# Kernel optimization log

Hardware: AMD Instinct MI355X
Metric: run time of the kernel (lower is better)

Reference implementation:

```python
import jax, jax.numpy as jnp
import numpy as np

N_NODES = 50000
N_EDGES = 800000
F_IN = 128
HEADS = 4
C_OUT = 32
NEG_SLOPE = 0.2
BN_EPS = 1e-5


def _add_self_loops(edge_index, edge_attr, n):
    # PyG fill_value='mean': self-loop attr = mean of incoming edge attrs per node (0 if none)
    src, dst = edge_index[0], edge_index[1]
    deg = jax.ops.segment_sum(jnp.ones_like(edge_attr[:, 0]), dst, num_segments=n)
    loop_attr = jax.ops.segment_sum(edge_attr, dst, num_segments=n) / jnp.maximum(deg, 1.0)[:, None]
    loop = jnp.arange(n)
    src2 = jnp.concatenate([src, loop])
    dst2 = jnp.concatenate([dst, loop])
    attr2 = jnp.concatenate([edge_attr, loop_attr], axis=0)
    return src2, dst2, attr2


def _segment_softmax(logits, seg, n):
    m = jax.ops.segment_max(logits, seg, num_segments=n)
    m = jnp.where(jnp.isfinite(m), m, 0.0)
    ex = jnp.exp(logits - m[seg])
    s = jax.ops.segment_sum(ex, seg, num_segments=n)
    return ex / s[seg]


def _gatv2(x, src, dst, eattr, Wl, bl, Wr, br, We, att, bias, n):
    # x: [n, F]; returns [n, HEADS*C_OUT]
    xl = (x @ Wl + bl).reshape(n, HEADS, C_OUT)
    xr = (x @ Wr + br).reshape(n, HEADS, C_OUT)
    ea = (eattr @ We).reshape(-1, HEADS, C_OUT)
    xlj = xl[src]                                   # [E, H, C] gather
    msg = jax.nn.leaky_relu(xlj + xr[dst] + ea, NEG_SLOPE)
    logits = jnp.einsum('ehc,hc->eh', msg, att)     # [E, H]
    alpha = _segment_softmax(logits, dst, n)
    out = jax.ops.segment_sum(xlj * alpha[..., None], dst, num_segments=n)
    return out.reshape(n, HEADS * C_OUT) + bias


def _batchnorm(x, gamma, beta):
    mu = x.mean(axis=0)
    var = x.var(axis=0)
    return gamma * (x - mu) * jax.lax.rsqrt(var + BN_EPS) + beta


def setup_inputs() -> dict:
    key = jax.random.key(0)
    ks = jax.random.split(key, 20)
    HC = HEADS * C_OUT
    s = 0.05
    inp = {
        'emb': jax.random.normal(ks[0], (N_NODES, F_IN), dtype=jnp.float32),
        'edge_index': jax.random.randint(ks[1], (2, N_EDGES), 0, N_NODES, dtype=jnp.int64),
        'edge_weight': jax.random.uniform(ks[2], (N_EDGES, 1), dtype=jnp.float32),
        'Wl1': jax.random.normal(ks[3], (F_IN, HC)) * s,
        'bl1': jnp.zeros((HC,), jnp.float32),
        'Wr1': jax.random.normal(ks[4], (F_IN, HC)) * s,
        'br1': jnp.zeros((HC,), jnp.float32),
        'We1': jax.random.normal(ks[5], (1, HC)) * s,
        'att1': jax.random.normal(ks[6], (HEADS, C_OUT)) * s,
        'bias1': jnp.zeros((HC,), jnp.float32),
        'gamma1': jnp.ones((HC,), jnp.float32),
        'beta1': jnp.zeros((HC,), jnp.float32),
        'Wl2': jax.random.normal(ks[7], (HC, HC)) * s,
        'bl2': jnp.zeros((HC,), jnp.float32),
        'Wr2': jax.random.normal(ks[8], (HC, HC)) * s,
        'br2': jnp.zeros((HC,), jnp.float32),
        'We2': jax.random.normal(ks[9], (1, HC)) * s,
        'att2': jax.random.normal(ks[10], (HEADS, C_OUT)) * s,
        'bias2': jnp.zeros((HC,), jnp.float32),
    }
    return inp


def reference(emb, edge_index, edge_weight, Wl1, bl1, Wr1, br1, We1, att1, bias1,
              gamma1, beta1, Wl2, bl2, Wr2, br2, We2, att2, bias2):
    n = emb.shape[0]
    src, dst, eattr = _add_self_loops(edge_index, edge_weight, n)
    h1 = _gatv2(emb, src, dst, eattr, Wl1, bl1, Wr1, br1, We1, att1, bias1, n)
    h1 = jax.nn.elu(_batchnorm(h1, gamma1, beta1))
    h2 = _gatv2(h1, src, dst, eattr, Wl2, bl2, Wr2, br2, We2, att2, bias2, n)
    # fusion: mean over [input_emb, h1, h2] along stacked axis
    return (emb + h1 + h2) / 3.0
```

## Files before the change

kernel.cpp:

```cpp
#include <hip/hip_runtime.h>
#include <hip/hip_bf16.h>
#include <math.h>

#define N_NODES 50000
#define N_EDGES 800000
#define HC 128
#define SLOT 64

#define BM 128
#define NBX ((N_NODES + BM - 1) / BM)
#define NCHK 64
#define EPB (N_EDGES / NCHK)
#define NRNG 4
#define RNG_N (N_NODES / NRNG)
#define RNG_W (RNG_N / 2)
#define NW (N_NODES / 2)
#define NSCAT (NCHK * NRNG)

typedef short bh8 __attribute__((ext_vector_type(8)));
typedef float f4 __attribute__((ext_vector_type(4)));
typedef float f2 __attribute__((ext_vector_type(2)));

__device__ __forceinline__ unsigned int pk2(float a, float b) {
  return (unsigned int)__bfloat16_as_ushort(__float2bfloat16(a)) |
         ((unsigned int)__bfloat16_as_ushort(__float2bfloat16(b)) << 16);
}
__device__ __forceinline__ float blo(unsigned int u) { return __uint_as_float(u << 16); }
__device__ __forceinline__ float bhi(unsigned int u) { return __uint_as_float(u & 0xffff0000u); }
__device__ __forceinline__ f2 vmax2(f2 a, f2 b) {
#if __has_builtin(__builtin_elementwise_max)
  return __builtin_elementwise_max(a, b);
#else
  f2 r; r.x = fmaxf(a.x, b.x); r.y = fmaxf(a.y, b.y); return r;
#endif
}

__global__ __launch_bounds__(256) void k_histprep(
    const float* __restrict__ Wl1, const float* __restrict__ Wr1,
    const float* __restrict__ Wl2, const float* __restrict__ Wr2,
    unsigned short* __restrict__ WtAll,
    float* __restrict__ chsum, float* __restrict__ chsq,
    const int* __restrict__ ei, unsigned int* __restrict__ counts32) {
  __shared__ unsigned int hist[RNG_W];
  int tid = threadIdx.x, bid = blockIdx.x;
  int gid = bid * 256 + tid;
  {
    int m = gid >> 14;
    int idx = gid & 16383;
    const float* src = (m == 0) ? Wl1 : (m == 1) ? Wr1 : (m == 2) ? Wl2 : Wr2;
    int k = idx >> 7, n = idx & 127;
    WtAll[((size_t)m * HC + n) * HC + k] =
        __bfloat16_as_ushort(__float2bfloat16(src[k * HC + n]));
    if (gid < HC) { chsum[gid] = 0.f; chsq[gid] = 0.f; }
  }
  int c = bid >> 2, r = bid & 3;
  int rb = r * RNG_N;
  for (int w = tid; w < RNG_W; w += 256) hist[w] = 0u;
  __syncthreads();
  const int* dstp = ei + N_EDGES + c * EPB;
  for (int g = tid; g < EPB / 4; g += 256) {
    int4 d4 = *(const int4*)(dstp + g * 4);
    int dl;
    dl = d4.x - rb; if ((unsigned)dl < RNG_N) atomicAdd(&hist[dl >> 1], (dl & 1) ? 0x10000u : 1u);
    dl = d4.y - rb; if ((unsigned)dl < RNG_N) atomicAdd(&hist[dl >> 1], (dl & 1) ? 0x10000u : 1u);
    dl = d4.z - rb; if ((unsigned)dl < RNG_N) atomicAdd(&hist[dl >> 1], (dl & 1) ? 0x10000u : 1u);
    dl = d4.w - rb; if ((unsigned)dl < RNG_N) atomicAdd(&hist[dl >> 1], (dl & 1) ? 0x10000u : 1u);
  }
  __syncthreads();
  unsigned int* dst = counts32 + (size_t)c * NW + r * RNG_W;
  for (int w = tid; w < RNG_W; w += 256) dst[w] = hist[w];
}

__global__ __launch_bounds__(256) void k_scan(const unsigned int* __restrict__ counts32,
                                              unsigned int* __restrict__ bases32,
                                              int* __restrict__ cursor) {
  int w = blockIdx.x * 256 + threadIdx.x;
  if (w >= NW) return;
  unsigned int a0 = 0, a1 = 0;
#pragma unroll 4
  for (int b = 0; b < NCHK; ++b) {
    unsigned int v = counts32[(size_t)b * NW + w];
    bases32[(size_t)b * NW + w] = a0 | (a1 << 16);
    a0 += v & 0xffffu;
    a1 += v >> 16;
  }
  cursor[2 * w] = (int)a0;
  cursor[2 * w + 1] = (int)a1;
}

__global__ __launch_bounds__(256) void k_scat_g1(
    const int* __restrict__ ei, const float* __restrict__ ew,
    const unsigned int* __restrict__ bases32, unsigned int* __restrict__ slots,
    const float* __restrict__ X, const unsigned short* __restrict__ Wt,
    const float* __restrict__ b0, const float* __restrict__ b1,
    unsigned short* __restrict__ Y0b, float* __restrict__ Y1) {
  __shared__ __align__(16) unsigned int lsbuf[16384];
  int tid = threadIdx.x, bid = blockIdx.x;
  if (bid < NSCAT) {
    int c = bid >> 2, r = bid & 3;
    int rb = r * RNG_N;
    const unsigned int* bp = bases32 + (size_t)c * NW + r * RNG_W;
    for (int w = tid; w < RNG_W; w += 256) lsbuf[w] = bp[w];
    __syncthreads();
    const int* sp = ei + c * EPB;
    const int* dp = ei + N_EDGES + c * EPB;
    const float* wp = ew + c * EPB;
    for (int g = tid; g < EPB / 4; g += 256) {
      int4 s4 = *(const int4*)(sp + g * 4);
      int4 d4 = *(const int4*)(dp + g * 4);
      float4 w4 = *(const float4*)(wp + g * 4);
      int ss[4] = {s4.x, s4.y, s4.z, s4.w};
      int dd[4] = {d4.x, d4.y, d4.z, d4.w};
      float ww[4] = {w4.x, w4.y, w4.z, w4.w};
#pragma unroll
      for (int i = 0; i < 4; ++i) {
        int dl = dd[i] - rb;
        if ((unsigned)dl < RNG_N) {
          unsigned int old = atomicAdd(&lsbuf[dl >> 1], (dl & 1) ? 0x10000u : 1u);
          unsigned int pos = (dl & 1) ? (old >> 16) : (old & 0xffffu);
          unsigned int wq = min((unsigned int)(ww[i] * 65536.f + 0.5f), 65535u);
          if (pos < SLOT)
            slots[(size_t)dd[i] * SLOT + pos] = ((unsigned int)ss[i] << 16) | wq;
        }
      }
    }
    return;
  }
  unsigned short* Xls = (unsigned short*)lsbuf;
  unsigned short* Wls = Xls + 128 * 128;
  int row0 = (bid - NSCAT) * BM;
  {
    int r = tid >> 1;
    int ks = (tid & 1) * 64;
    int gr = row0 + r;
    const float* xp = X + (size_t)gr * HC + ks;
    int sw = r & 15;
#pragma unroll
    for (int i = 0; i < 4; ++i) {
      float f[16];
      if (gr < N_NODES) {
        *(float4*)&f[0] = *(const float4*)(xp + i * 16);
        *(float4*)&f[4] = *(const float4*)(xp + i * 16 + 4);
        *(float4*)&f[8] = *(const float4*)(xp + i * 16 + 8);
        *(float4*)&f[12] = *(const float4*)(xp + i * 16 + 12);
      } else {
#pragma unroll
        for (int j = 0; j < 16; ++j) f[j] = 0.f;
      }
      int kg = (ks >> 3) + i * 2;
      *(uint4*)&Xls[r * 128 + ((kg ^ sw) * 8)] =
          make_uint4(pk2(f[0], f[1]), pk2(f[2], f[3]), pk2(f[4], f[5]), pk2(f[6], f[7]));
      *(uint4*)&Xls[r * 128 + (((kg + 1) ^ sw) * 8)] =
          make_uint4(pk2(f[8], f[9]), pk2(f[10], f[11]), pk2(f[12], f[13]), pk2(f[14], f[15]));
    }
  }
  int lane = tid & 63;
  int wv = tid >> 6;
  int lrow = lane & 15;
  int lq = lane >> 4;
  int rbase = wv * 32;
#pragma unroll
  for (int half = 0; half < 2; ++half) {
    if (half) __syncthreads();
    {
      int n = tid >> 1;
      int ks2 = (tid & 1) * 64;
      const unsigned short* wp = Wt + half * (HC * HC) + n * HC + ks2;
      int swn = n & 15;
#pragma unroll
      for (int g = 0; g < 8; ++g) {
        uint4 v = *(const uint4*)(wp + g * 8);
        int kg = (ks2 >> 3) + g;
        *(uint4*)&Wls[n * 128 + ((kg ^ swn) * 8)] = v;
      }
    }
    __syncthreads();
    f4 acc[2][8];
#pragma unroll
    for (int mt = 0; mt < 2; ++mt)
#pragma unroll
      for (int nt = 0; nt < 8; ++nt) acc[mt][nt] = (f4){0.f, 0.f, 0.f, 0.f};
#pragma unroll
    for (int kk = 0; kk < 4; ++kk) {
      int kg = kk * 4 + lq;
      bh8 a0 = *(const bh8*)&Xls[(rbase + lrow) * 128 + ((kg ^ lrow) * 8)];
      bh8 a1 = *(const bh8*)&Xls[(rbase + 16 + lrow) * 128 + ((kg ^ lrow) * 8)];
#pragma unroll
      for (int nt = 0; nt < 8; ++nt) {
        bh8 b = *(const bh8*)&Wls[(nt * 16 + lrow) * 128 + ((kg ^ lrow) * 8)];
        acc[0][nt] = __builtin_amdgcn_mfma_f32_16x16x32_bf16(a0, b, acc[0][nt], 0, 0, 0);
        acc[1][nt] = __builtin_amdgcn_mfma_f32_16x16x32_bf16(a1, b, acc[1][nt], 0, 0, 0);
      }
    }
    const float* bb = half ? b1 : b0;
    float bv[8];
#pragma unroll
    for (int nt = 0; nt < 8; ++nt) bv[nt] = bb[nt * 16 + lrow];
#pragma unroll
    for (int mt = 0; mt < 2; ++mt) {
#pragma unroll
      for (int rr = 0; rr < 4; ++rr) {
        int gr = row0 + rbase + mt * 16 + lq * 4 + rr;
        if (gr < N_NODES) {
          if (half == 0) {
#pragma unroll
            for (int nt = 0; nt < 8; ++nt)
              Y0b[(size_t)gr * HC + nt * 16 + lrow] =
                  __bfloat16_as_ushort(__float2bfloat16(acc[mt][nt][rr] + bv[nt]));
          } else {
#pragma unroll
            for (int nt = 0; nt < 8; ++nt)
              Y1[(size_t)gr * HC + nt * 16 + lrow] = acc[mt][nt][rr] + bv[nt];
          }
        }
      }
    }
  }
}

__global__ __launch_bounds__(256) void k_gemm2(
    const unsigned short* __restrict__ Xb, const unsigned short* __restrict__ Wt,
    const float* __restrict__ b0, const float* __restrict__ b1,
    unsigned char* __restrict__ Y0f8, float* __restrict__ Y1,
    const float* __restrict__ chsum, const float* __restrict__ chsq,
    const float* __restrict__ gamma, const float* __restrict__ beta) {
  __shared__ __align__(16) unsigned short Xls[128 * 128];
  __shared__ __align__(16) unsigned short Wls[128 * 128];
  __shared__ float ssc[HC], ssh[HC];
  int tid = threadIdx.x;
  if (tid < HC) {
    float mu = chsum[tid] * (1.f / N_NODES);
    float var = chsq[tid] * (1.f / N_NODES) - mu * mu;
    float sc = gamma[tid] * rsqrtf(var + 1e-5f);
    ssc[tid] = sc;
    ssh[tid] = beta[tid] - mu * sc;
  }
  __syncthreads();
  int row0 = blockIdx.x * BM;
  {
    int r = tid >> 1;
    int ks = (tid & 1) * 64;
    int gr = row0 + r;
    const unsigned short* xp = Xb + (size_t)gr * HC + ks;
    int sw = r & 15;
#pragma unroll
    for (int i = 0; i < 4; ++i) {
      float f[16];
      if (gr < N_NODES) {
        uint4 ua = *(const uint4*)(xp + i * 16);
        uint4 ub = *(const uint4*)(xp + i * 16 + 8);
        f[0] = blo(ua.x); f[1] = bhi(ua.x); f[2] = blo(ua.y); f[3] = bhi(ua.y);
        f[4] = blo(ua.z); f[5] = bhi(ua.z); f[6] = blo(ua.w); f[7] = bhi(ua.w);
        f[8] = blo(ub.x); f[9] = bhi(ub.x); f[10] = blo(ub.y); f[11] = bhi(ub.y);
        f[12] = blo(ub.z); f[13] = bhi(ub.z); f[14] = blo(ub.w); f[15] = bhi(ub.w);
      } else {
#pragma unroll
        for (int j = 0; j < 16; ++j) f[j] = 0.f;
      }
#pragma unroll
      for (int j = 0; j < 16; ++j) {
        float y = fmaf(f[j], ssc[ks + i * 16 + j], ssh[ks + i * 16 + j]);
        f[j] = (y > 0.f) ? y : (__expf(y) - 1.f);
      }
      int kg = (ks >> 3) + i * 2;
      *(uint4*)&Xls[r * 128 + ((kg ^ sw) * 8)] =
          make_uint4(pk2(f[0], f[1]), pk2(f[2], f[3]), pk2(f[4], f[5]), pk2(f[6], f[7]));
      *(uint4*)&Xls[r * 128 + (((kg + 1) ^ sw) * 8)] =
          make_uint4(pk2(f[8], f[9]), pk2(f[10], f[11]), pk2(f[12], f[13]), pk2(f[14], f[15]));
    }
  }
  int lane = tid & 63;
  int wv = tid >> 6;
  int lrow = lane & 15;
  int lq = lane >> 4;
  int rbase = wv * 32;
#pragma unroll
  for (int half = 0; half < 2; ++half) {
    if (half) __syncthreads();
    {
      int n = tid >> 1;
      int ks = (tid & 1) * 64;
      const unsigned short* wp = Wt + half * (HC * HC) + n * HC + ks;
      int swn = n & 15;
#pragma unroll
      for (int g = 0; g < 8; ++g) {
        uint4 v = *(const uint4*)(wp + g * 8);
        int kg = (ks >> 3) + g;
        *(uint4*)&Wls[n * 128 + ((kg ^ swn) * 8)] = v;
      }
    }
    __syncthreads();
    f4 acc[2][8];
#pragma unroll
    for (int mt = 0; mt < 2; ++mt)
#pragma unroll
      for (int nt = 0; nt < 8; ++nt) acc[mt][nt] = (f4){0.f, 0.f, 0.f, 0.f};
#pragma unroll
    for (int kk = 0; kk < 4; ++kk) {
      int kg = kk * 4 + lq;
      bh8 a0 = *(const bh8*)&Xls[(rbase + lrow) * 128 + ((kg ^ lrow) * 8)];
      bh8 a1 = *(const bh8*)&Xls[(rbase + 16 + lrow) * 128 + ((kg ^ lrow) * 8)];
#pragma unroll
      for (int nt = 0; nt < 8; ++nt) {
        bh8 b = *(const bh8*)&Wls[(nt * 16 + lrow) * 128 + ((kg ^ lrow) * 8)];
        acc[0][nt] = __builtin_amdgcn_mfma_f32_16x16x32_bf16(a0, b, acc[0][nt], 0, 0, 0);
        acc[1][nt] = __builtin_amdgcn_mfma_f32_16x16x32_bf16(a1, b, acc[1][nt], 0, 0, 0);
      }
    }
    const float* bb = half ? b1 : b0;
    float bv[8];
#pragma unroll
    for (int nt = 0; nt < 8; ++nt) bv[nt] = bb[nt * 16 + lrow];
#pragma unroll
    for (int mt = 0; mt < 2; ++mt) {
#pragma unroll
      for (int rr = 0; rr < 4; ++rr) {
        int gr = row0 + rbase + mt * 16 + lq * 4 + rr;
        if (gr < N_NODES) {
          if (half == 0) {
#pragma unroll
            for (int nt = 0; nt < 8; ++nt) {
              float v = acc[mt][nt][rr] + bv[nt];
              int p = __builtin_amdgcn_cvt_pk_fp8_f32(v, v, 0, false);
              Y0f8[(size_t)gr * HC + nt * 16 + lrow] = (unsigned char)(p & 0xff);
            }
          } else {
#pragma unroll
            for (int nt = 0; nt < 8; ++nt)
              Y1[(size_t)gr * HC + nt * 16 + lrow] = acc[mt][nt][rr] + bv[nt];
          }
        }
      }
    }
  }
}

template <int FINAL, int F8>
__global__ __launch_bounds__(256) void k_gat(
    const void* __restrict__ xlv, const float* __restrict__ xr,
    const int* __restrict__ cursor, const unsigned int* __restrict__ slots,
    const float* __restrict__ We, const float* __restrict__ att,
    const float* __restrict__ bias, void* __restrict__ out,
    const float* __restrict__ emb, const unsigned short* __restrict__ h1p,
    const float* __restrict__ chsum, const float* __restrict__ chsq,
    const float* __restrict__ gamma, const float* __restrict__ beta) {
  int g = threadIdx.x >> 5;
  int lane = threadIdx.x & 31;
  int n = blockIdx.x * 8 + g;
  int fi = n * 32 + lane;
  const uint2* xl2 = (const uint2*)xlv;
  const unsigned int* xf = (const unsigned int*)xlv;
  float4 xr4 = ((const float4*)xr)[fi];
  float4 we4 = ((const float4*)We)[lane];
  float4 at4 = ((const float4*)att)[lane];
  const float LOG2E = 1.4426950408889634f;
  f2 xr01 = {xr4.x, xr4.y}, xr23 = {xr4.z, xr4.w};
  f2 we01 = {we4.x, we4.y}, we23 = {we4.z, we4.w};
  f2 at01 = {at4.x * LOG2E, at4.y * LOG2E}, at23 = {at4.z * LOG2E, at4.w * LOG2E};
  int deg = min(cursor[n], SLOT);
  int base = n * SLOT;
  int deg32 = min(deg, 32);

  unsigned int ev = (lane < deg32) ? slots[base + lane] : 0u;
  float evw = (float)(ev & 0xffffu) * (1.f / 65536.f);
  float wsum = evw;
#pragma unroll
  for (int m = 16; m >= 1; m >>= 1) wsum += __shfl_xor(wsum, m);

  float l = 0.f;
  f2 o01 = {0.f, 0.f}, o23 = {0.f, 0.f};

  auto decode = [&](uint2 gc, f2& a, f2& b) {
    if (F8) {
      a = __builtin_amdgcn_cvt_pk_f32_fp8((int)gc.x, false);
      b = __builtin_amdgcn_cvt_pk_f32_fp8((int)gc.x, true);
    } else {
      a = (f2){blo(gc.x), bhi(gc.x)};
      b = (f2){blo(gc.y), bhi(gc.y)};
    }
  };
  auto edge_body = [&](float w, uint2 gc, bool valid) {
    f2 a, b;
    decode(gc, a, b);
    f2 m01 = (a + xr01) + w * we01;
    f2 m23 = (b + xr23) + w * we23;
    m01 = vmax2(m01, m01 * 0.2f);
    m23 = vmax2(m23, m23 * 0.2f);
    f2 dp = m01 * at01 + m23 * at23;
    float p = dp.x + dp.y;
    p += __shfl_xor(p, 1);
    p += __shfl_xor(p, 2);
    p += __shfl_xor(p, 4);
#if __has_builtin(__builtin_amdgcn_exp2f)
    float e = valid ? __builtin_amdgcn_exp2f(p) : 0.f;
#else
    float e = valid ? __expf(p * 0.6931471805599453f) : 0.f;
#endif
    l += e;
    o01 = o01 + e * a;
    o23 = o23 + e * b;
  };
  auto fetch = [&](int j, uint2& qq, float& ww) {
    int jc = min(j, deg32 - 1);
    unsigned int evj = __shfl(ev, jc, 32);
    ww = (float)(evj & 0xffffu) * (1.f / 65536.f);
    int s = (int)(evj >> 16);
    if (F8) qq.x = xf[s * 32 + lane];
    else qq = xl2[s * 32 + lane];
  };

  if (deg32 > 0) {
    uint2 q0, q1, q2, q3;
    float w0, w1, w2, w3;
    fetch(0, q0, w0);
    fetch(1, q1, w1);
    fetch(2, q2, w2);
    fetch(3, q3, w3);
    for (int b = 0; b < deg32; b += 4) {
      uint2 c0 = q0, c1 = q1, c2 = q2, c3 = q3;
      float x0 = w0, x1 = w1, x2 = w2, x3 = w3;
      fetch(b + 4, q0, w0);
      fetch(b + 5, q1, w1);
      fetch(b + 6, q2, w2);
      fetch(b + 7, q3, w3);
      edge_body(x0, c0, true);
      edge_body(x1, c1, b + 1 < deg32);
      edge_body(x2, c2, b + 2 < deg32);
      edge_body(x3, c3, b + 3 < deg32);
    }
  }
  if (deg > 32) {
    for (int j = base + 32; j < base + deg; ++j) {
      unsigned int evj = slots[j];
      float w = (float)(evj & 0xffffu) * (1.f / 65536.f);
      wsum += w;
      int s = (int)(evj >> 16);
      uint2 gc;
      if (F8) gc.x = xf[s * 32 + lane];
      else gc = xl2[s * 32 + lane];
      edge_body(w, gc, true);
    }
  }
  {
    float wself = (deg > 0) ? wsum / (float)deg : 0.f;
    uint2 gs;
    if (F8) gs.x = xf[n * 32 + lane];
    else gs = xl2[n * 32 + lane];
    edge_body(wself, gs, true);
  }

  float inv = 1.f / l;
  float4 o = make_float4(o01.x, o01.y, o23.x, o23.y);
  float4 b4 = ((const float4*)bias)[lane];
  float4 r;
  r.x = fmaf(o.x, inv, b4.x);
  r.y = fmaf(o.y, inv, b4.y);
  r.z = fmaf(o.z, inv, b4.z);
  r.w = fmaf(o.w, inv, b4.w);
  if (FINAL) {
    float4 e4 = ((const float4*)emb)[fi];
    uint2 hh = ((const uint2*)h1p)[fi];
    float4 h4;
    h4.x = blo(hh.x); h4.y = bhi(hh.x); h4.z = blo(hh.y); h4.w = bhi(hh.y);
    float4 cs = ((const float4*)chsum)[lane];
    float4 cq = ((const float4*)chsq)[lane];
    float4 gm = ((const float4*)gamma)[lane];
    float4 bt = ((const float4*)beta)[lane];
    const float invN = 1.f / N_NODES;
    float4 sc4, sh4;
    {
      float mu = cs.x * invN, var = cq.x * invN - mu * mu;
      sc4.x = gm.x * rsqrtf(var + 1e-5f); sh4.x = bt.x - mu * sc4.x;
      mu = cs.y * invN; var = cq.y * invN - mu * mu;
      sc4.y = gm.y * rsqrtf(var + 1e-5f); sh4.y = bt.y - mu * sc4.y;
      mu = cs.z * invN; var = cq.z * invN - mu * mu;
      sc4.z = gm.z * rsqrtf(var + 1e-5f); sh4.z = bt.z - mu * sc4.z;
      mu = cs.w * invN; var = cq.w * invN - mu * mu;
      sc4.w = gm.w * rsqrtf(var + 1e-5f); sh4.w = bt.w - mu * sc4.w;
    }
    float4 h;
    h.x = fmaf(h4.x, sc4.x, sh4.x);
    h.y = fmaf(h4.y, sc4.y, sh4.y);
    h.z = fmaf(h4.z, sc4.z, sh4.z);
    h.w = fmaf(h4.w, sc4.w, sh4.w);
    h.x = (h.x > 0.f) ? h.x : (__expf(h.x) - 1.f);
    h.y = (h.y > 0.f) ? h.y : (__expf(h.y) - 1.f);
    h.z = (h.z > 0.f) ? h.z : (__expf(h.z) - 1.f);
    h.w = (h.w > 0.f) ? h.w : (__expf(h.w) - 1.f);
    const float k3 = 1.f / 3.f;
    r.x = (e4.x + h.x + r.x) * k3;
    r.y = (e4.y + h.y + r.y) * k3;
    r.z = (e4.z + h.z + r.z) * k3;
    r.w = (e4.w + h.w + r.w) * k3;
    ((float4*)out)[fi] = r;
  } else {
    ((uint2*)out)[fi] = make_uint2(pk2(r.x, r.y), pk2(r.z, r.w));
  }
}

#define BN_ROWS 200
__global__ __launch_bounds__(256) void k_bnstats(const unsigned short* __restrict__ h1b,
                                                 float* __restrict__ chsum,
                                                 float* __restrict__ chsq) {
  int c2 = threadIdx.x & 63;
  int g = threadIdx.x >> 6;
  int r0 = blockIdx.x * BN_ROWS;
  float s0 = 0.f, s1 = 0.f, q0 = 0.f, q1 = 0.f;
  const unsigned int* h32 = (const unsigned int*)h1b;
  for (int r = r0 + g; r < r0 + BN_ROWS; r += 4) {
    unsigned int u = h32[(size_t)r * 64 + c2];
    float a = blo(u), b = bhi(u);
    s0 += a; q0 += a * a;
    s1 += b; q1 += b * b;
  }
  __shared__ float sh[256][4];
  sh[threadIdx.x][0] = s0; sh[threadIdx.x][1] = q0;
  sh[threadIdx.x][2] = s1; sh[threadIdx.x][3] = q1;
  __syncthreads();
  if (g == 0) {
    float ts0 = 0.f, tq0 = 0.f, ts1 = 0.f, tq1 = 0.f;
#pragma unroll
    for (int gg = 0; gg < 4; ++gg) {
      ts0 += sh[gg * 64 + c2][0]; tq0 += sh[gg * 64 + c2][1];
      ts1 += sh[gg * 64 + c2][2]; tq1 += sh[gg * 64 + c2][3];
    }
    atomicAdd(chsum + 2 * c2, ts0);
    atomicAdd(chsq + 2 * c2, tq0);
    atomicAdd(chsum + 2 * c2 + 1, ts1);
    atomicAdd(chsq + 2 * c2 + 1, tq1);
  }
}

extern "C" void kernel_launch(void* const* d_in, const int* in_sizes, int n_in,
                              void* d_out, int out_size, void* d_ws, size_t ws_size,
                              hipStream_t stream) {
  const float* emb = (const float*)d_in[0];
  const int* ei = (const int*)d_in[1];
  const float* ew = (const float*)d_in[2];
  const float* Wl1 = (const float*)d_in[3];
  const float* bl1 = (const float*)d_in[4];
  const float* Wr1 = (const float*)d_in[5];
  const float* br1 = (const float*)d_in[6];
  const float* We1 = (const float*)d_in[7];
  const float* att1 = (const float*)d_in[8];
  const float* bias1 = (const float*)d_in[9];
  const float* gamma1 = (const float*)d_in[10];
  const float* beta1 = (const float*)d_in[11];
  const float* Wl2 = (const float*)d_in[12];
  const float* bl2 = (const float*)d_in[13];
  const float* Wr2 = (const float*)d_in[14];
  const float* br2 = (const float*)d_in[15];
  const float* We2 = (const float*)d_in[16];
  const float* att2 = (const float*)d_in[17];
  const float* bias2 = (const float*)d_in[18];
  float* out = (float*)d_out;

  char* wsb = (char*)d_ws;
  size_t off = 0;
  auto alloc = [&](size_t bytes) -> void* {
    void* p = (void*)(wsb + off);
    off += (bytes + 255) & ~(size_t)255;
    return p;
  };
  int* cursor = (int*)alloc((size_t)N_NODES * 4);
  float* chsum = (float*)alloc(HC * 4);
  float* chsq = (float*)alloc(HC * 4);
  unsigned short* WtAll = (unsigned short*)alloc((size_t)4 * HC * HC * 2);
  unsigned int* counts32 = (unsigned int*)alloc((size_t)NCHK * NW * 4);
  unsigned int* bases32 = (unsigned int*)alloc((size_t)NCHK * NW * 4);
  unsigned int* slots = (unsigned int*)alloc((size_t)N_NODES * SLOT * 4);
  unsigned short* xlb = (unsigned short*)alloc((size_t)N_NODES * HC * 2);
  unsigned char* xlf8 = (unsigned char*)alloc((size_t)N_NODES * HC);
  float* xr = (float*)alloc((size_t)N_NODES * HC * 4);
  unsigned short* h1b = (unsigned short*)alloc((size_t)N_NODES * HC * 2);

  k_histprep<<<NSCAT, 256, 0, stream>>>(Wl1, Wr1, Wl2, Wr2, WtAll, chsum, chsq,
                                        ei, counts32);
  k_scan<<<(NW + 255) / 256, 256, 0, stream>>>(counts32, bases32, cursor);
  k_scat_g1<<<NSCAT + NBX, 256, 0, stream>>>(ei, ew, bases32, slots, emb, WtAll,
                                             bl1, br1, xlb, xr);
  k_gat<0, 0><<<N_NODES / 8, 256, 0, stream>>>(xlb, xr, cursor, slots, We1, att1,
                                               bias1, (void*)h1b, nullptr, nullptr,
                                               nullptr, nullptr, nullptr, nullptr);
  k_bnstats<<<N_NODES / BN_ROWS, 256, 0, stream>>>(h1b, chsum, chsq);
  k_gemm2<<<NBX, 256, 0, stream>>>(h1b, WtAll + 2 * HC * HC, bl2, br2, xlf8, xr,
                                   chsum, chsq, gamma1, beta1);
  k_gat<1, 1><<<N_NODES / 8, 256, 0, stream>>>(xlf8, xr, cursor, slots, We2, att2,
                                               bias2, (void*)out, emb, h1b,
                                               chsum, chsq, gamma1, beta1);
}
```

Measured before the change: 278.6 us.

## Schedule GAT nodes sorted by degree to balance warp work

Builds a per-block degree histogram during the scan, prefix-sums it in a new single-block kernel, and fills a node permutation sorted by degree inside extra blocks of the scatter kernel. Both GAT kernels now look up their node through this permutation, so the eight node groups in a block have similar degrees and loop trip counts. This is meant to cut divergence and tail imbalance within a block. It also folds the 1/65536 edge-weight scale into We to save a multiply per edge. The cost is an extra launch, extra passes, and less locality for xr and output accesses, since neighbouring blocks no longer handle neighbouring nodes.

```diff
diff --git a/kernel.cpp b/kernel.cpp
--- a/kernel.cpp
+++ b/kernel.cpp
@@ -16,6 +16,7 @@
 #define RNG_W (RNG_N / 2)
 #define NW (N_NODES / 2)
 #define NSCAT (NCHK * NRNG)
+#define NB2 ((NW + 255) / 256)
 
 typedef short bh8 __attribute__((ext_vector_type(8)));
 typedef float f4 __attribute__((ext_vector_type(4)));
@@ -73,19 +74,50 @@
 
 __global__ __launch_bounds__(256) void k_scan(const unsigned int* __restrict__ counts32,
                                               unsigned int* __restrict__ bases32,
-                                              int* __restrict__ cursor) {
-  int w = blockIdx.x * 256 + threadIdx.x;
-  if (w >= NW) return;
-  unsigned int a0 = 0, a1 = 0;
+                                              int* __restrict__ cursor,
+                                              int* __restrict__ counts2) {
+  __shared__ int dh[80];
+  int tid = threadIdx.x;
+  int w = blockIdx.x * 256 + tid;
+  if (tid < 80) dh[tid] = 0;
+  __syncthreads();
+  if (w < NW) {
+    unsigned int a0 = 0, a1 = 0;
 #pragma unroll 4
-  for (int b = 0; b < NCHK; ++b) {
-    unsigned int v = counts32[(size_t)b * NW + w];
-    bases32[(size_t)b * NW + w] = a0 | (a1 << 16);
-    a0 += v & 0xffffu;
-    a1 += v >> 16;
-  }
-  cursor[2 * w] = (int)a0;
-  cursor[2 * w + 1] = (int)a1;
+    for (int b = 0; b < NCHK; ++b) {
+      unsigned int v = counts32[(size_t)b * NW + w];
+      bases32[(size_t)b * NW + w] = a0 | (a1 << 16);
+      a0 += v & 0xffffu;
+      a1 += v >> 16;
+    }
+    cursor[2 * w] = (int)a0;
+    cursor[2 * w + 1] = (int)a1;
+    atomicAdd(&dh[min((int)a0, SLOT)], 1);
+    atomicAdd(&dh[min((int)a1, SLOT)], 1);
+  }
+  __syncthreads();
+  if (tid <= SLOT) counts2[blockIdx.x * 72 + tid] = dh[tid];
+}
+
+__global__ __launch_bounds__(256) void k_dprefix(const int* __restrict__ counts2,
+                                                 int* __restrict__ bases2) {
+  __shared__ int colsum[80], cbase[80];
+  int d = threadIdx.x;
+  if (d <= SLOT) {
+    int s = 0;
+    for (int b = 0; b < NB2; ++b) s += counts2[b * 72 + d];
+    colsum[d] = s;
+  }
+  __syncthreads();
+  if (d == 0) {
+    int a = 0;
+    for (int i = 0; i <= SLOT; ++i) { cbase[i] = a; a += colsum[i]; }
+  }
+  __syncthreads();
+  if (d <= SLOT) {
+    int a = cbase[d];
+    for (int b = 0; b < NB2; ++b) { bases2[b * 72 + d] = a; a += counts2[b * 72 + d]; }
+  }
 }
 
 __global__ __launch_bounds__(256) void k_scat_g1(
@@ -93,9 +125,26 @@
     const unsigned int* __restrict__ bases32, unsigned int* __restrict__ slots,
     const float* __restrict__ X, const unsigned short* __restrict__ Wt,
     const float* __restrict__ b0, const float* __restrict__ b1,
-    unsigned short* __restrict__ Y0b, float* __restrict__ Y1) {
+    unsigned short* __restrict__ Y0b, float* __restrict__ Y1,
+    const int* __restrict__ cursor, const int* __restrict__ bases2,
+    int* __restrict__ perm) {
   __shared__ __align__(16) unsigned int lsbuf[16384];
   int tid = threadIdx.x, bid = blockIdx.x;
+  if (bid >= NSCAT + NBX) {
+    int b2 = bid - NSCAT - NBX;
+    int* dcur = (int*)lsbuf;
+    if (tid <= SLOT) dcur[tid] = bases2[b2 * 72 + tid];
+    __syncthreads();
+    for (int i = tid; i < 512; i += 256) {
+      int nn = b2 * 512 + i;
+      if (nn < N_NODES) {
+        int d = min(cursor[nn], SLOT);
+        int pos = atomicAdd(&dcur[d], 1);
+        perm[pos] = nn;
+      }
+    }
+    return;
+  }
   if (bid < NSCAT) {
     int c = bid >> 2, r = bid & 3;
     int rb = r * RNG_N;
@@ -339,6 +388,7 @@
 __global__ __launch_bounds__(256) void k_gat(
     const void* __restrict__ xlv, const float* __restrict__ xr,
     const int* __restrict__ cursor, const unsigned int* __restrict__ slots,
+    const int* __restrict__ perm,
     const float* __restrict__ We, const float* __restrict__ att,
     const float* __restrict__ bias, void* __restrict__ out,
     const float* __restrict__ emb, const unsigned short* __restrict__ h1p,
@@ -346,7 +396,7 @@
     const float* __restrict__ gamma, const float* __restrict__ beta) {
   int g = threadIdx.x >> 5;
   int lane = threadIdx.x & 31;
-  int n = blockIdx.x * 8 + g;
+  int n = perm[blockIdx.x * 8 + g];
   int fi = n * 32 + lane;
   const uint2* xl2 = (const uint2*)xlv;
   const unsigned int* xf = (const unsigned int*)xlv;
@@ -354,16 +404,16 @@
   float4 we4 = ((const float4*)We)[lane];
   float4 at4 = ((const float4*)att)[lane];
   const float LOG2E = 1.4426950408889634f;
+  const float WSC = 1.f / 65536.f;
   f2 xr01 = {xr4.x, xr4.y}, xr23 = {xr4.z, xr4.w};
-  f2 we01 = {we4.x, we4.y}, we23 = {we4.z, we4.w};
+  f2 we01 = {we4.x * WSC, we4.y * WSC}, we23 = {we4.z * WSC, we4.w * WSC};
   f2 at01 = {at4.x * LOG2E, at4.y * LOG2E}, at23 = {at4.z * LOG2E, at4.w * LOG2E};
   int deg = min(cursor[n], SLOT);
   int base = n * SLOT;
   int deg32 = min(deg, 32);
 
   unsigned int ev = (lane < deg32) ? slots[base + lane] : 0u;
-  float evw = (float)(ev & 0xffffu) * (1.f / 65536.f);
-  float wsum = evw;
+  float wsum = (float)(ev & 0xffffu);
 #pragma unroll
   for (int m = 16; m >= 1; m >>= 1) wsum += __shfl_xor(wsum, m);
 
@@ -403,7 +453,7 @@
   auto fetch = [&](int j, uint2& qq, float& ww) {
     int jc = min(j, deg32 - 1);
     unsigned int evj = __shfl(ev, jc, 32);
-    ww = (float)(evj & 0xffffu) * (1.f / 65536.f);
+    ww = (float)(evj & 0xffffu);
     int s = (int)(evj >> 16);
     if (F8) qq.x = xf[s * 32 + lane];
     else qq = xl2[s * 32 + lane];
@@ -432,7 +482,7 @@
   if (deg > 32) {
     for (int j = base + 32; j < base + deg; ++j) {
       unsigned int evj = slots[j];
-      float w = (float)(evj & 0xffffu) * (1.f / 65536.f);
+      float w = (float)(evj & 0xffffu);
       wsum += w;
       int s = (int)(evj >> 16);
       uint2 gc;
@@ -573,19 +623,25 @@
   unsigned char* xlf8 = (unsigned char*)alloc((size_t)N_NODES * HC);
   float* xr = (float*)alloc((size_t)N_NODES * HC * 4);
   unsigned short* h1b = (unsigned short*)alloc((size_t)N_NODES * HC * 2);
+  int* counts2 = (int*)alloc((size_t)NB2 * 72 * 4);
+  int* bases2 = (int*)alloc((size_t)NB2 * 72 * 4);
+  int* perm = (int*)alloc((size_t)N_NODES * 4);
 
   k_histprep<<<NSCAT, 256, 0, stream>>>(Wl1, Wr1, Wl2, Wr2, WtAll, chsum, chsq,
                                         ei, counts32);
-  k_scan<<<(NW + 255) / 256, 256, 0, stream>>>(counts32, bases32, cursor);
-  k_scat_g1<<<NSCAT + NBX, 256, 0, stream>>>(ei, ew, bases32, slots, emb, WtAll,
-                                             bl1, br1, xlb, xr);
-  k_gat<0, 0><<<N_NODES / 8, 256, 0, stream>>>(xlb, xr, cursor, slots, We1, att1,
-                                               bias1, (void*)h1b, nullptr, nullptr,
-                                               nullptr, nullptr, nullptr, nullptr);
+  k_scan<<<NB2, 256, 0, stream>>>(counts32, bases32, cursor, counts2);
+  k_dprefix<<<1, 256, 0, stream>>>(counts2, bases2);
+  k_scat_g1<<<NSCAT + NBX + NB2, 256, 0, stream>>>(ei, ew, bases32, slots, emb,
+                                                   WtAll, bl1, br1, xlb, xr,
+                                                   cursor, bases2, perm);
+  k_gat<0, 0><<<N_NODES / 8, 256, 0, stream>>>(xlb, xr, cursor, slots, perm, We1,
+                                               att1, bias1, (void*)h1b, nullptr,
+                                               nullptr, nullptr, nullptr, nullptr,
+                                               nullptr);
   k_bnstats<<<N_NODES / BN_ROWS, 256, 0, stream>>>(h1b, chsum, chsq);
   k_gemm2<<<NBX, 256, 0, stream>>>(h1b, WtAll + 2 * HC * HC, bl2, br2, xlf8, xr,
                                    chsum, chsq, gamma1, beta1);
-  k_gat<1, 1><<<N_NODES / 8, 256, 0, stream>>>(xlf8, xr, cursor, slots, We2, att2,
-                                               bias2, (void*)out, emb, h1b,
+  k_gat<1, 1><<<N_NODES / 8, 256, 0, stream>>>(xlf8, xr, cursor, slots, perm, We2,
+                                               att2, bias2, (void*)out, emb, h1b,
                                                chsum, chsq, gamma1, beta1);
 }
```

Measured after the change: 278.3 us. Within noise of the previous version (-0.1%).
